# Performance work log

Measured on AMD Instinct MI355X. Metric: run time of the kernel, lower is better.

Reference implementation:

```python
import jax, jax.numpy as jnp
import numpy as np

N_HEADS = 2
OUT_DIM = 128
HEAD_DIM = OUT_DIM // N_HEADS
LN_EPS = 1e-5


def setup_inputs() -> dict:
    key = jax.random.key(0)
    ks = jax.random.split(key, 12)
    B, N = 8192, 32
    node_dim, edge_dim, time_dim = 172, 172, 100
    s_q = (node_dim + time_dim) ** -0.5
    s_kv = (node_dim + edge_dim + time_dim) ** -0.5
    s_o = OUT_DIM ** -0.5
    return {
        "node_feat": jax.random.normal(ks[0], (B, node_dim), jnp.float32),
        "time_feat": jax.random.normal(ks[1], (B, time_dim), jnp.float32),
        "edge_feat": jax.random.normal(ks[2], (B, N, edge_dim), jnp.float32),
        "nbr_node_feat": jax.random.normal(ks[3], (B, N, node_dim), jnp.float32),
        "nbr_time_feat": jax.random.normal(ks[4], (B, N, time_dim), jnp.float32),
        "nbr_mask": jax.random.randint(ks[5], (B, N), 0, 2, jnp.int32),
        "Wq": jax.random.normal(ks[6], (OUT_DIM, node_dim + time_dim), jnp.float32) * s_q,
        "bq": jnp.zeros((OUT_DIM,), jnp.float32),
        "Wkv": jax.random.normal(ks[7], (2 * OUT_DIM, node_dim + edge_dim + time_dim), jnp.float32) * s_kv,
        "bkv": jnp.zeros((2 * OUT_DIM,), jnp.float32),
        "Wo": jax.random.normal(ks[8], (OUT_DIM, OUT_DIM), jnp.float32) * s_o,
        "bo": jnp.zeros((OUT_DIM,), jnp.float32),
        "gamma": jnp.ones((OUT_DIM,), jnp.float32),
        "beta": jnp.zeros((OUT_DIM,), jnp.float32),
    }


def reference(node_feat, time_feat, edge_feat, nbr_node_feat, nbr_time_feat,
              nbr_mask, Wq, bq, Wkv, bkv, Wo, bo, gamma, beta):
    B = node_feat.shape[0]
    # Q projection: [B, out_dim]
    Q = jnp.concatenate([node_feat, time_feat], axis=-1) @ Wq.T + bq
    # KV projection: [B, N, 2*out_dim]
    Z = jnp.concatenate([nbr_node_feat, edge_feat, nbr_time_feat], axis=-1) @ Wkv.T + bkv
    # NOTE: faithful to torch: plain reshape of [B, N, out_dim] -> [B, H, N, d]
    # (mixes neighbor/head axes; identical row-major semantics in jnp)
    K = Z[:, :, :OUT_DIM].reshape(B, N_HEADS, -1, HEAD_DIM)
    V = Z[:, :, OUT_DIM:].reshape(B, N_HEADS, -1, HEAD_DIM)
    Qh = Q.reshape(B, N_HEADS, 1, HEAD_DIM)
    A = jnp.einsum('bhld,bhnd->bhln', Qh, K) * (HEAD_DIM ** -0.5)  # [B,H,1,N]
    pad = (nbr_mask == 0).reshape(B, 1, 1, -1)
    A = jnp.where(pad, jnp.float32(-1e10), A)
    A = jax.nn.softmax(A, axis=-1)  # dropout is identity at inference
    O = jnp.einsum('bhln,bhnd->bhld', A, V).reshape(B, OUT_DIM)
    out = O @ Wo.T + bo
    mu = jnp.mean(out, axis=-1, keepdims=True)
    var = jnp.mean(jnp.square(out - mu), axis=-1, keepdims=True)
    return (out - mu) * jax.lax.rsqrt(var + LN_EPS) * gamma + beta
```

## Files before the change

kernel.cpp:

```cpp
#include <hip/hip_runtime.h>
#include <hip/hip_bf16.h>

typedef __attribute__((ext_vector_type(4))) float f32x4;
typedef __attribute__((ext_vector_type(8))) short short8;
typedef __attribute__((ext_vector_type(8))) __bf16 bf16x8;

#define NDIM 172
#define EDIM 172
#define TDIM 100
#define KCAT 444
#define QDIM 272
#define ODIM 128
#define ZDIM 256
#define NNBR 32
#define NPH 14
#define NT 7
#define RPB 32
#define LN_EPS 1e-5f

#define Z_OFF    0
#define A_OFF    65536
#define QRES_OFF 81920
#define MASK_OFF 98304
#define PB_OFF   102400
#define OB_OFF   103424
#define RED_OFF  105472
#define SMEM_BYTES 105600

#define ZB(r,c) ((((r) * 512) + ((c) * 2)) ^ (((r) & 7) << 4))

#define BARRIER() do { \
    asm volatile("s_waitcnt lgkmcnt(0)\ns_barrier" ::: "memory"); \
    __builtin_amdgcn_sched_barrier(0); \
} while (0)

__device__ __forceinline__ unsigned short f2bf(float f) {
    unsigned u = __builtin_bit_cast(unsigned, f);
    u += 0x7fffu + ((u >> 16) & 1u);
    return (unsigned short)(u >> 16);
}
__device__ __forceinline__ float bf2f(unsigned short h) {
    unsigned u = ((unsigned)h) << 16;
    return __builtin_bit_cast(float, u);
}
__device__ __forceinline__ unsigned short bfb(float f) {
    return __builtin_bit_cast(unsigned short, (__bf16)f);
}

#define WFRAG_N (NPH * 8192)
#define WQT_N (QDIM * ODIM)
#define WOT_N (ODIM * ODIM)
__global__ void prep_pack(const float* __restrict__ Wkv, const float* __restrict__ Wq,
                          const float* __restrict__ Wo,
                          unsigned short* __restrict__ wfrag,
                          unsigned short* __restrict__ wqT,
                          unsigned short* __restrict__ woT) {
    int idx = blockIdx.x * 256 + threadIdx.x;
    if (idx < WFRAG_N) {
        int phase = idx >> 13;
        int r = idx & 8191;
        int n16 = r >> 9;
        int q = r & 511;
        int l = q >> 3, e = q & 7;
        int row = n16 * 16 + (l & 15);
        int k = phase * 32 + ((l >> 4) << 3) + e;
        wfrag[idx] = f2bf(k < KCAT ? Wkv[row * KCAT + k] : 0.f);
    } else if (idx < WFRAG_N + WQT_N) {
        int j = idx - WFRAG_N;
        int k = j >> 7, c = j & 127;
        wqT[j] = f2bf(Wq[c * QDIM + k]);
    } else if (idx < WFRAG_N + WQT_N + WOT_N) {
        int j = idx - WFRAG_N - WQT_N;
        int k = j >> 7, c = j & 127;
        woT[j] = f2bf(Wo[c * ODIM + k]);
    }
}

__global__ __launch_bounds__(256) void q_proj(
    const float* __restrict__ node_feat, const float* __restrict__ time_feat,
    const unsigned short* __restrict__ wqT, const float* __restrict__ bq,
    float* __restrict__ Qbuf) {
    __shared__ float x[8][QDIM];
    const int tid = threadIdx.x;
    const long b0 = (long)blockIdx.x * 8;
    for (int g = tid; g < 8 * QDIM; g += 256) {
        int r = g / QDIM, k = g - r * QDIM;
        x[r][k] = (k < NDIM) ? node_feat[(b0 + r) * NDIM + k]
                             : time_feat[(b0 + r) * TDIM + (k - NDIM)];
    }
    __syncthreads();
    const int c = tid & 127;
    const int rb = (tid >> 7) * 4;
    float s0 = bq[c], s1 = s0, s2 = s0, s3 = s0;
    #pragma unroll 8
    for (int k = 0; k < QDIM; k++) {
        float w = bf2f(wqT[k * 128 + c]);
        s0 += x[rb + 0][k] * w;
        s1 += x[rb + 1][k] * w;
        s2 += x[rb + 2][k] * w;
        s3 += x[rb + 3][k] * w;
    }
    Qbuf[(b0 + rb + 0) * 128 + c] = s0;
    Qbuf[(b0 + rb + 1) * 128 + c] = s1;
    Qbuf[(b0 + rb + 2) * 128 + c] = s2;
    Qbuf[(b0 + rb + 3) * 128 + c] = s3;
}

__global__ __launch_bounds__(512, 2) void ta_fused(
    const float* __restrict__ edge_feat, const float* __restrict__ nbr_node,
    const float* __restrict__ nbr_time, const int* __restrict__ nbr_mask,
    const float* __restrict__ Qbuf,
    const unsigned short* __restrict__ wfrag, const float* __restrict__ bkv,
    const unsigned short* __restrict__ woT, const float* __restrict__ bo,
    const float* __restrict__ gamma, const float* __restrict__ beta,
    float* __restrict__ out)
{
    extern __shared__ __align__(16) unsigned char smem[];
    float* qresL = (float*)(smem + QRES_OFF);
    int*   maskL = (int*)(smem + MASK_OFF);
    float* Pband = (float*)(smem + PB_OFF);
    float* Obuf  = (float*)(smem + OB_OFF);
    float* red   = (float*)(smem + RED_OFF);

    const int tid  = threadIdx.x;
    const int lane = tid & 63;
    const int wid  = tid >> 6;
    const int b0   = blockIdx.x * RPB;

    for (int i = tid; i < RPB * NNBR; i += 512)
        maskL[i] = nbr_mask[(long)b0 * NNBR + i];
    for (int i = tid; i < RPB * ODIM; i += 512)
        qresL[i] = Qbuf[(long)b0 * ODIM + i];
    __syncthreads();

    bf16x8 Wr[2 * NPH];
    #pragma unroll
    for (int p = 0; p < NPH; p++)
        #pragma unroll
        for (int j = 0; j < 2; j++)
            Wr[p * 2 + j] = __builtin_bit_cast(bf16x8,
                *(const short8*)(wfrag + ((size_t)(p * 16 + wid * 2 + j) * 512 + lane * 8)));
    const float bk0 = bkv[wid * 32 + (lane & 15)];
    const float bk1 = bkv[wid * 32 + 16 + (lane & 15)];

    const int rowA  = tid >> 4;
    const int kgrp4 = (tid & 15) * 4;
    const int awb   = ((rowA * 128 + (tid & 15) * 8) ^ ((rowA & 7) << 4));

    const float* aptr[NT];
    int astr[NT];
    #pragma unroll
    for (int t = 0; t < NT; t++) {
        int k = t * 64 + kgrp4;
        long rg = (long)b0 * NNBR + rowA;
        if (k < NDIM) {
            aptr[t] = nbr_node + rg * NDIM + k;
            astr[t] = NNBR * NDIM;
        } else if (k < NDIM + EDIM) {
            aptr[t] = edge_feat + rg * EDIM + (k - NDIM);
            astr[t] = NNBR * EDIM;
        } else {
            int off = k - NDIM - EDIM;
            if (off > TDIM - 4) off = TDIM - 4;
            aptr[t] = nbr_time + rg * TDIM + off;
            astr[t] = NNBR * TDIM;
        }
    }

    float4 rs[NT];
    #pragma unroll
    for (int t = 0; t < NT; t++) {
        rs[t] = *(const float4*)aptr[t];
        aptr[t] += astr[t];
    }
    __builtin_amdgcn_sched_barrier(0);

    for (int ri = 0; ri < RPB; ri++) {
        const int tb = ri * NT;
        f32x4 acc[2][2];
        #pragma unroll
        for (int m = 0; m < 2; m++)
            #pragma unroll
            for (int n = 0; n < 2; n++) acc[m][n] = (f32x4){0.f, 0.f, 0.f, 0.f};

        #pragma unroll
        for (int w = 0; w < 4; w++) {
            const int t0 = w * 2;
            unsigned char* aw0 = smem + A_OFF + (((tb + t0) & 3) << 12);
            unsigned char* aw1 = smem + A_OFF + (((tb + t0 + 1) & 3) << 12);
            {
                float4 v = rs[t0];
                uint2 u;
                u.x = (unsigned)bfb(v.x) | ((unsigned)bfb(v.y) << 16);
                u.y = (unsigned)bfb(v.z) | ((unsigned)bfb(v.w) << 16);
                *(uint2*)(aw0 + awb) = u;
            }
            if (t0 + 1 < NT) {
                float4 v = rs[t0 + 1];
                uint2 u;
                u.x = (unsigned)bfb(v.x) | ((unsigned)bfb(v.y) << 16);
                u.y = (unsigned)bfb(v.z) | ((unsigned)bfb(v.w) << 16);
                *(uint2*)(aw1 + awb) = u;
            }
            if (ri + 1 < RPB) {
                rs[t0] = *(const float4*)aptr[t0];
                aptr[t0] += astr[t0];
                if (t0 + 1 < NT) {
                    rs[t0 + 1] = *(const float4*)aptr[t0 + 1];
                    aptr[t0 + 1] += astr[t0 + 1];
                }
            }
            __builtin_amdgcn_sched_barrier(0);
            BARRIER();
            __builtin_amdgcn_s_setprio(1);
            #pragma unroll
            for (int tt = 0; tt < 2; tt++) {
                if (t0 + tt < NT) {
                    const unsigned char* aw = tt ? aw1 : aw0;
                    #pragma unroll
                    for (int kk = 0; kk < 2; kk++) {
                        bf16x8 af[2];
                        #pragma unroll
                        for (int m = 0; m < 2; m++) {
                            int row = m * 16 + (lane & 15);
                            af[m] = __builtin_bit_cast(bf16x8, *(const short8*)(
                                aw + row * 128 + ((kk * 64 + (lane >> 4) * 16) ^ ((row & 7) << 4))));
                        }
                        const int p = (t0 + tt) * 2 + kk;
                        acc[0][0] = __builtin_amdgcn_mfma_f32_16x16x32_bf16(af[0], Wr[p*2+0], acc[0][0], 0, 0, 0);
                        acc[0][1] = __builtin_amdgcn_mfma_f32_16x16x32_bf16(af[0], Wr[p*2+1], acc[0][1], 0, 0, 0);
                        acc[1][0] = __builtin_amdgcn_mfma_f32_16x16x32_bf16(af[1], Wr[p*2+0], acc[1][0], 0, 0, 0);
                        acc[1][1] = __builtin_amdgcn_mfma_f32_16x16x32_bf16(af[1], Wr[p*2+1], acc[1][1], 0, 0, 0);
                    }
                }
            }
            __builtin_amdgcn_s_setprio(0);
        }

        const int gi = ri & 3;
        #pragma unroll
        for (int n = 0; n < 2; n++) {
            int col = wid * 32 + n * 16 + (lane & 15);
            float bk = n ? bk1 : bk0;
            #pragma unroll
            for (int m = 0; m < 2; m++)
                #pragma unroll
                for (int j = 0; j < 4; j++) {
                    int rowZ = gi * 32 + m * 16 + (lane >> 4) * 4 + j;
                    *(unsigned short*)(smem + ZB(rowZ, col)) = bfb(acc[m][n][j] + bk);
                }
        }

        if (gi == 3) {
            const int g = ri >> 2;
            BARRIER();

            {
                int bl = wid >> 1, h = wid & 1;
                int n2 = lane >> 1, half = lane & 1;
                int np = h * 16 + (n2 >> 1);
                int rowZ = bl * NNBR + np;
                int cb = (n2 & 1) * 64 + half * 32;
                const float* q = qresL + (g * 4 + bl) * ODIM + h * 64 + half * 32;
                float s = 0.f;
                #pragma unroll
                for (int j = 0; j < 4; j++) {
                    short8 z8 = *(const short8*)(smem + ZB(rowZ, cb + j * 8));
                    #pragma unroll
                    for (int e = 0; e < 8; e++)
                        s += q[j * 8 + e] * bf2f((unsigned short)z8[e]);
                }
                s += __shfl_xor(s, 1);
                s *= 0.125f;
                if (maskL[(g * 4 + bl) * NNBR + n2] == 0) s = -1e10f;
                float mx = s;
                #pragma unroll
                for (int off = 1; off < 64; off <<= 1) mx = fmaxf(mx, __shfl_xor(mx, off));
                float e = __expf(s - mx);
                float sum = e;
                #pragma unroll
                for (int off = 1; off < 64; off <<= 1) sum += __shfl_xor(sum, off);
                float pv = e * 2.f / sum;
                if (half == 0) Pband[(bl * 2 + h) * NNBR + n2] = pv;
            }
            BARRIER();

            {
                int b = tid >> 7, c = tid & 127, h = c >> 6, d = c & 63;
                const float* P = Pband + (b * 2 + h) * NNBR;
                float s = 0.f;
                #pragma unroll
                for (int n2 = 0; n2 < NNBR; n2++) {
                    int np = h * 16 + (n2 >> 1);
                    int col = ODIM + (n2 & 1) * 64 + d;
                    s += P[n2] * bf2f(*(const unsigned short*)(smem + ZB(b * NNBR + np, col)));
                }
                Obuf[b * ODIM + c] = s;
            }
            BARRIER();

            {
                int b = tid >> 7, c = tid & 127;
                float s = bo[c];
                const float* ob = Obuf + b * ODIM;
                #pragma unroll 8
                for (int k = 0; k < ODIM; k++)
                    s += ob[k] * bf2f(woT[k * 128 + c]);
                float s1 = s, s2 = s * s;
                #pragma unroll
                for (int off = 1; off < 64; off <<= 1) {
                    s1 += __shfl_xor(s1, off);
                    s2 += __shfl_xor(s2, off);
                }
                if (lane == 0) { red[wid * 2] = s1; red[wid * 2 + 1] = s2; }
                BARRIER();
                float t1 = red[b * 4 + 0] + red[b * 4 + 2];
                float t2 = red[b * 4 + 1] + red[b * 4 + 3];
                float mu  = t1 * (1.f / 128.f);
                float var = t2 * (1.f / 128.f) - mu * mu;
                float inv = rsqrtf(var + LN_EPS);
                out[(long)(b0 + g * 4 + b) * ODIM + c] = (s - mu) * inv * gamma[c] + beta[c];
            }
            BARRIER();
        }
    }
}

extern "C" void kernel_launch(void* const* d_in, const int* in_sizes, int n_in,
                              void* d_out, int out_size, void* d_ws, size_t ws_size,
                              hipStream_t stream) {
    const float* node_feat = (const float*)d_in[0];
    const float* time_feat = (const float*)d_in[1];
    const float* edge_feat = (const float*)d_in[2];
    const float* nbr_node  = (const float*)d_in[3];
    const float* nbr_time  = (const float*)d_in[4];
    const int*   nbr_mask  = (const int*)d_in[5];
    const float* Wq   = (const float*)d_in[6];
    const float* bq   = (const float*)d_in[7];
    const float* Wkv  = (const float*)d_in[8];
    const float* bkv  = (const float*)d_in[9];
    const float* Wo   = (const float*)d_in[10];
    const float* bo   = (const float*)d_in[11];
    const float* gma  = (const float*)d_in[12];
    const float* bta  = (const float*)d_in[13];
    float* out = (float*)d_out;

    const int B = in_sizes[0] / NDIM;

    char* ws = (char*)d_ws;
    float* Qbuf = (float*)ws;
    unsigned short* wfrag = (unsigned short*)(ws + (size_t)B * ODIM * 4);
    unsigned short* wqT   = wfrag + WFRAG_N;
    unsigned short* woT   = wqT + WQT_N;

    hipFuncSetAttribute((const void*)ta_fused,
                        hipFuncAttributeMaxDynamicSharedMemorySize, SMEM_BYTES);

    const int prep_total = WFRAG_N + WQT_N + WOT_N;
    prep_pack<<<dim3((prep_total + 255) / 256), dim3(256), 0, stream>>>(
        Wkv, Wq, Wo, wfrag, wqT, woT);
    q_proj<<<dim3(B / 8), dim3(256), 0, stream>>>(node_feat, time_feat, wqT, bq, Qbuf);
    ta_fused<<<dim3(B / RPB), dim3(512), SMEM_BYTES, stream>>>(
        edge_feat, nbr_node, nbr_time, nbr_mask, Qbuf,
        wfrag, bkv, woT, bo, gma, bta, out);
}
```

Measured before the change: 173.5 us.

## Stage four A tiles per barrier and cache Wo in LDS

The K-loop now stages four A sub-tiles per barrier instead of two, using an 8-slot LDS ring, which halves the barriers per row. The bf16 Wo^T matrix (32 KB) is also copied into LDS once per block, so the output projection reads it from shared memory rather than global memory. LDS use grows from about 105 KB to about 155 KB per block. With launch bounds of 2 blocks per CU, that may no longer fit and could drop occupancy to one block per CU.

```diff
diff --git a/kernel.cpp b/kernel.cpp
--- a/kernel.cpp
+++ b/kernel.cpp
@@ -20,12 +20,13 @@
 
 #define Z_OFF    0
 #define A_OFF    65536
-#define QRES_OFF 81920
-#define MASK_OFF 98304
-#define PB_OFF   102400
-#define OB_OFF   103424
-#define RED_OFF  105472
-#define SMEM_BYTES 105600
+#define WOT_OFF  98304
+#define QRES_OFF 131072
+#define MASK_OFF 147456
+#define PB_OFF   151552
+#define OB_OFF   152576
+#define RED_OFF  154624
+#define SMEM_BYTES 154752
 
 #define ZB(r,c) ((((r) * 512) + ((c) * 2)) ^ (((r) & 7) << 4))
 
@@ -121,6 +122,7 @@
     float* Pband = (float*)(smem + PB_OFF);
     float* Obuf  = (float*)(smem + OB_OFF);
     float* red   = (float*)(smem + RED_OFF);
+    unsigned short* woL = (unsigned short*)(smem + WOT_OFF);
 
     const int tid  = threadIdx.x;
     const int lane = tid & 63;
@@ -131,6 +133,9 @@
         maskL[i] = nbr_mask[(long)b0 * NNBR + i];
     for (int i = tid; i < RPB * ODIM; i += 512)
         qresL[i] = Qbuf[(long)b0 * ODIM + i];
+    #pragma unroll
+    for (int i = 0; i < 4; i++)
+        ((uint4*)woL)[i * 512 + tid] = ((const uint4*)woT)[i * 512 + tid];
     __syncthreads();
 
     bf16x8 Wr[2 * NPH];
@@ -184,39 +189,39 @@
             for (int n = 0; n < 2; n++) acc[m][n] = (f32x4){0.f, 0.f, 0.f, 0.f};
 
         #pragma unroll
-        for (int w = 0; w < 4; w++) {
-            const int t0 = w * 2;
-            unsigned char* aw0 = smem + A_OFF + (((tb + t0) & 3) << 12);
-            unsigned char* aw1 = smem + A_OFF + (((tb + t0 + 1) & 3) << 12);
-            {
-                float4 v = rs[t0];
-                uint2 u;
-                u.x = (unsigned)bfb(v.x) | ((unsigned)bfb(v.y) << 16);
-                u.y = (unsigned)bfb(v.z) | ((unsigned)bfb(v.w) << 16);
-                *(uint2*)(aw0 + awb) = u;
-            }
-            if (t0 + 1 < NT) {
-                float4 v = rs[t0 + 1];
-                uint2 u;
-                u.x = (unsigned)bfb(v.x) | ((unsigned)bfb(v.y) << 16);
-                u.y = (unsigned)bfb(v.z) | ((unsigned)bfb(v.w) << 16);
-                *(uint2*)(aw1 + awb) = u;
+        for (int w = 0; w < 2; w++) {
+            const int t0 = w * 4;
+            const int ntw = w ? 3 : 4;
+            #pragma unroll
+            for (int tt = 0; tt < 4; tt++) {
+                if (tt < ntw) {
+                    const int t = t0 + tt;
+                    unsigned char* aw = smem + A_OFF + (((tb + t) & 7) << 12);
+                    float4 v = rs[t];
+                    uint2 u;
+                    u.x = (unsigned)bfb(v.x) | ((unsigned)bfb(v.y) << 16);
+                    u.y = (unsigned)bfb(v.z) | ((unsigned)bfb(v.w) << 16);
+                    *(uint2*)(aw + awb) = u;
+                }
             }
             if (ri + 1 < RPB) {
-                rs[t0] = *(const float4*)aptr[t0];
-                aptr[t0] += astr[t0];
-                if (t0 + 1 < NT) {
-                    rs[t0 + 1] = *(const float4*)aptr[t0 + 1];
-                    aptr[t0 + 1] += astr[t0 + 1];
+                #pragma unroll
+                for (int tt = 0; tt < 4; tt++) {
+                    if (tt < ntw) {
+                        const int t = t0 + tt;
+                        rs[t] = *(const float4*)aptr[t];
+                        aptr[t] += astr[t];
+                    }
                 }
             }
             __builtin_amdgcn_sched_barrier(0);
             BARRIER();
             __builtin_amdgcn_s_setprio(1);
             #pragma unroll
-            for (int tt = 0; tt < 2; tt++) {
-                if (t0 + tt < NT) {
-                    const unsigned char* aw = tt ? aw1 : aw0;
+            for (int tt = 0; tt < 4; tt++) {
+                if (tt < ntw) {
+                    const int t = t0 + tt;
+                    const unsigned char* aw = smem + A_OFF + (((tb + t) & 7) << 12);
                     #pragma unroll
                     for (int kk = 0; kk < 2; kk++) {
                         bf16x8 af[2];
@@ -226,7 +231,7 @@
                             af[m] = __builtin_bit_cast(bf16x8, *(const short8*)(
                                 aw + row * 128 + ((kk * 64 + (lane >> 4) * 16) ^ ((row & 7) << 4))));
                         }
-                        const int p = (t0 + tt) * 2 + kk;
+                        const int p = t * 2 + kk;
                         acc[0][0] = __builtin_amdgcn_mfma_f32_16x16x32_bf16(af[0], Wr[p*2+0], acc[0][0], 0, 0, 0);
                         acc[0][1] = __builtin_amdgcn_mfma_f32_16x16x32_bf16(af[0], Wr[p*2+1], acc[0][1], 0, 0, 0);
                         acc[1][0] = __builtin_amdgcn_mfma_f32_16x16x32_bf16(af[1], Wr[p*2+0], acc[1][0], 0, 0, 0);
@@ -305,7 +310,7 @@
                 const float* ob = Obuf + b * ODIM;
                 #pragma unroll 8
                 for (int k = 0; k < ODIM; k++)
-                    s += ob[k] * bf2f(woT[k * 128 + c]);
+                    s += ob[k] * bf2f(woL[k * 128 + c]);
                 float s1 = s, s2 = s * s;
                 #pragma unroll
                 for (int off = 1; off < 64; off <<= 1) {
```

Result: faster. 153.3 us (-11.6%).
